# Optimization experiments

Measured on AMD Instinct MI355X. Metric: run time of the kernel, lower is better.

Reference implementation:

```python
import jax, jax.numpy as jnp
import numpy as np

B, T, I, H, L = 64, 512, 256, 512, 2


def setup_inputs() -> dict:
    key = jax.random.key(0)
    ks = jax.random.split(key, 9)
    std = 1.0 / np.sqrt(H)  # matches reset_parameters uniform(-std, std)
    u = lambda k, shape: jax.random.uniform(k, shape, jnp.float32, -std, std)
    return {
        "x": jax.random.normal(ks[0], (B, T, I), jnp.float32),
        "w_xh0": u(ks[1], (4 * H, I)),  "b_xh0": u(ks[2], (4 * H,)),
        "w_hh0": u(ks[3], (4 * H, H)), "b_hh0": u(ks[4], (4 * H,)),
        "w_xh1": u(ks[5], (4 * H, H)), "b_xh1": u(ks[6], (4 * H,)),
        "w_hh1": u(ks[7], (4 * H, H)), "b_hh1": u(ks[8], (4 * H,)),
    }


def _cell(x, h, c, Wx, bx, Wh, bh):
    # gates = xh(x) + hh(h); chunk order: input, forget, cell, output
    gates = x @ Wx.T + bx + h @ Wh.T + bh
    i, f, g, o = jnp.split(gates, 4, axis=1)
    cy = c * jax.nn.sigmoid(f) + jax.nn.sigmoid(i) * jnp.tanh(g)
    hy = jax.nn.sigmoid(o) * jnp.tanh(cy)
    return hy, cy


def reference(x, w_xh0, b_xh0, w_hh0, b_hh0, w_xh1, b_xh1, w_hh1, b_hh1):
    Bx, Tx, _ = x.shape
    Hx = w_hh0.shape[1]
    params = [(w_xh0, b_xh0, w_hh0, b_hh0), (w_xh1, b_xh1, w_hh1, b_hh1)]
    h0 = jnp.zeros((len(params), Bx, Hx), x.dtype)
    c0 = jnp.zeros((len(params), Bx, Hx), x.dtype)

    def step(carry, xt):
        h, c = carry
        inp = xt
        hs, cs = [], []
        for l, (Wx, bx, Wh, bh) in enumerate(params):
            hy, cy = _cell(inp, h[l], c[l], Wx, bx, Wh, bh)
            hs.append(hy)
            cs.append(cy)
            inp = hy  # dropout p=0.0 -> identity
        return (jnp.stack(hs), jnp.stack(cs)), inp

    (hT, cT), outs = jax.lax.scan(step, (h0, c0), jnp.swapaxes(x, 0, 1))
    return jnp.swapaxes(outs, 0, 1), (hT, cT)
```

## Files before the change

kernel.cpp:

```cpp
#include <hip/hip_runtime.h>
#include <stdint.h>

#define Bn 64
#define Tn 512
#define In 256
#define Hn 512
#define NBLK 64
#define OUT_HT 16777216
#define OUT_CT 16842752
#define LDS_BYTES 131072
#define SLOT_ELEMS (Bn * Hn)
#define DONE_WORDS (2 * 4 * Tn * 32)
#define DONE_BYTES (DONE_WORDS * 4)


typedef __attribute__((ext_vector_type(8))) short bf16x8;
typedef __attribute__((ext_vector_type(4))) float f32x4;
typedef unsigned long long u64;

__device__ __forceinline__ unsigned short f2bf(float f) {
    unsigned u = __float_as_uint(f);
    return (unsigned short)((u + 0x7fffu + ((u >> 16) & 1u)) >> 16);
}
__device__ __forceinline__ float sigm(float v) { return 1.0f / (1.0f + __expf(-v)); }
__device__ __forceinline__ float tanhv(float v) { float e = __expf(2.0f * v); return 1.0f - 2.0f / (e + 1.0f); }

__device__ __forceinline__ void stg_coh(unsigned short* p, unsigned short v) {
    __hip_atomic_store(p, v, __ATOMIC_RELAXED, __HIP_MEMORY_SCOPE_AGENT);
}
__device__ __forceinline__ int ld_cnt(const int* p) {
    return __hip_atomic_load(p, __ATOMIC_RELAXED, __HIP_MEMORY_SCOPE_AGENT);
}
__device__ __forceinline__ void st_flag(int* p, int v) {
    __hip_atomic_store(p, v, __ATOMIC_RELAXED, __HIP_MEMORY_SCOPE_AGENT);
}
__device__ __forceinline__ bf16x8 asbf(f32x4 v) {
    union { f32x4 f; bf16x8 h; } u; u.f = v; return u.h;
}

#define GLD16_ISSUE(A, VA)                                             \
  asm volatile(                                                        \
    "global_load_dwordx4 %0,  %16, off offset:0 sc0 sc1\n\t"          \
    "global_load_dwordx4 %1,  %16, off offset:64 sc0 sc1\n\t"         \
    "global_load_dwordx4 %2,  %16, off offset:128 sc0 sc1\n\t"        \
    "global_load_dwordx4 %3,  %16, off offset:192 sc0 sc1\n\t"        \
    "global_load_dwordx4 %4,  %16, off offset:256 sc0 sc1\n\t"        \
    "global_load_dwordx4 %5,  %16, off offset:320 sc0 sc1\n\t"        \
    "global_load_dwordx4 %6,  %16, off offset:384 sc0 sc1\n\t"        \
    "global_load_dwordx4 %7,  %16, off offset:448 sc0 sc1\n\t"        \
    "global_load_dwordx4 %8,  %16, off offset:512 sc0 sc1\n\t"        \
    "global_load_dwordx4 %9,  %16, off offset:576 sc0 sc1\n\t"        \
    "global_load_dwordx4 %10, %16, off offset:640 sc0 sc1\n\t"        \
    "global_load_dwordx4 %11, %16, off offset:704 sc0 sc1\n\t"        \
    "global_load_dwordx4 %12, %16, off offset:768 sc0 sc1\n\t"        \
    "global_load_dwordx4 %13, %16, off offset:832 sc0 sc1\n\t"        \
    "global_load_dwordx4 %14, %16, off offset:896 sc0 sc1\n\t"        \
    "global_load_dwordx4 %15, %16, off offset:960 sc0 sc1"             \
    : "=&v"(A[0]), "=&v"(A[1]), "=&v"(A[2]), "=&v"(A[3]),              \
      "=&v"(A[4]), "=&v"(A[5]), "=&v"(A[6]), "=&v"(A[7]),              \
      "=&v"(A[8]), "=&v"(A[9]), "=&v"(A[10]), "=&v"(A[11]),            \
      "=&v"(A[12]), "=&v"(A[13]), "=&v"(A[14]), "=&v"(A[15])           \
    : "v"(VA) : "memory")

#define VMW(n) do {                                                    \
    asm volatile("s_waitcnt vmcnt(" #n ")" ::: "memory");              \
    __builtin_amdgcn_sched_barrier(0);                                 \
  } while (0)

__global__ void lstm_prep(u64* __restrict__ z0, u64* __restrict__ z1,
                          int* __restrict__ dn) {
    int tid = blockIdx.x * blockDim.x + threadIdx.x;
    int stride = gridDim.x * blockDim.x;
    for (int i = tid; i < DONE_WORDS; i += stride) st_flag(dn + i, 0);
    for (int i = tid; i < SLOT_ELEMS / 4; i += stride) {
        __hip_atomic_store(z0 + i, (u64)0, __ATOMIC_RELAXED, __HIP_MEMORY_SCOPE_AGENT);
        __hip_atomic_store(z1 + i, (u64)0, __ATOMIC_RELAXED, __HIP_MEMORY_SCOPE_AGENT);
    }
}

__launch_bounds__(256, 1)
__global__ void lstm_main(const float* __restrict__ x,
                          const float* __restrict__ wxh0, const float* __restrict__ whh0,
                          const float* __restrict__ wxh1, const float* __restrict__ whh1,
                          const float* __restrict__ bx0, const float* __restrict__ bh0,
                          const float* __restrict__ bx1, const float* __restrict__ bh1,
                          float* __restrict__ out,
                          unsigned short* __restrict__ h0b,
                          unsigned short* __restrict__ h1b,
                          int* __restrict__ done, int nslot) {
    extern __shared__ char smem[];
    const int layer = blockIdx.x >> 5;
    const int cb    = blockIdx.x & 31;
    const int wv    = threadIdx.x >> 6;
    const int lane  = threadIdx.x & 63;
    const int quad  = lane >> 4;
    const int ln    = lane & 15;
    const int row0  = wv << 4;
    const int colh  = (cb << 4) + ln;

    const int I0 = (layer == 0) ? 8 : 16;
    const int K0 = (layer == 0) ? In : Hn;
    const float* Wxs = (layer == 0) ? wxh0 : wxh1;
    const float* Whs = (layer == 0) ? whh0 : whh1;
    u64* sm64 = (u64*)smem;
    const int tot0 = I0 * 4 * 64;
    for (int c = threadIdx.x; c < tot0; c += 256) {
        int lc = c & 63, qg = (c >> 6) & 3, ii = c >> 8;
        const float* src = Wxs + (size_t)(qg * Hn + (cb << 4) + (lc & 15)) * K0
                               + ii * 32 + (lc >> 4) * 8;
        f32x4 s0 = *(const f32x4*)src;
        f32x4 s1 = *(const f32x4*)(src + 4);
        u64 lo = (u64)f2bf(s0[0]) | ((u64)f2bf(s0[1]) << 16) |
                 ((u64)f2bf(s0[2]) << 32) | ((u64)f2bf(s0[3]) << 48);
        u64 hi = (u64)f2bf(s1[0]) | ((u64)f2bf(s1[1]) << 16) |
                 ((u64)f2bf(s1[2]) << 32) | ((u64)f2bf(s1[3]) << 48);
        sm64[c * 2] = lo; sm64[c * 2 + 1] = hi;
    }
    const int hbase = tot0;
    for (int c = threadIdx.x; c < 16 * 4 * 64; c += 256) {
        int lc = c & 63, qg = (c >> 6) & 3, ii = c >> 8;
        const float* src = Whs + (size_t)(qg * Hn + (cb << 4) + (lc & 15)) * Hn
                               + ii * 32 + (lc >> 4) * 8;
        f32x4 s0 = *(const f32x4*)src;
        f32x4 s1 = *(const f32x4*)(src + 4);
        u64 lo = (u64)f2bf(s0[0]) | ((u64)f2bf(s0[1]) << 16) |
                 ((u64)f2bf(s0[2]) << 32) | ((u64)f2bf(s0[3]) << 48);
        u64 hi = (u64)f2bf(s1[0]) | ((u64)f2bf(s1[1]) << 16) |
                 ((u64)f2bf(s1[2]) << 32) | ((u64)f2bf(s1[3]) << 48);
        sm64[(hbase + c) * 2] = lo; sm64[(hbase + c) * 2 + 1] = hi;
    }
    __syncthreads();
    const bf16x8* bfr = (const bf16x8*)smem;

    float bias[4];
#pragma unroll
    for (int q = 0; q < 4; ++q) {
        int gc = q * Hn + colh;
        bias[q] = (layer == 0) ? (bx0[gc] + bh0[gc]) : (bx1[gc] + bh1[gc]);
    }

    const float* xrow0 = x + (size_t)(row0 + ln) * Tn * In + quad * 8;
    const int hoff = (row0 + ln) * Hn + quad * 8;

    const int lm = lane & 31;
    const int* d0 = done + ((0 * 4 + wv) * Tn) * 32 + lm;
    const int* d1 = done + ((1 * 4 + wv) * Tn) * 32 + lm;
    int* pub = done + ((layer * 4 + wv) * Tn) * 32 + cb;

    float c[4] = {0.f, 0.f, 0.f, 0.f};
    int rs = 0, wsl = 1;
    int gdone = -1;

    for (int t = 0; t < Tn; ++t) {
        f32x4 acc[4];
#pragma unroll
        for (int q = 0; q < 4; ++q) acc[q] = (f32x4){bias[q], bias[q], bias[q], bias[q]};

        if (layer == 0) {
            const float* xp = xrow0 + (size_t)t * In;
            f32x4 xr[16];
#pragma unroll
            for (int i = 0; i < 8; ++i) {
                xr[2 * i]     = *(const f32x4*)(xp + i * 32);
                xr[2 * i + 1] = *(const f32x4*)(xp + i * 32 + 4);
            }
            bf16x8 axc[8];
#pragma unroll
            for (int i = 0; i < 8; ++i) {
                f32x4 xa = xr[2 * i], xc = xr[2 * i + 1];
                axc[i][0] = (short)f2bf(xa[0]); axc[i][1] = (short)f2bf(xa[1]);
                axc[i][2] = (short)f2bf(xa[2]); axc[i][3] = (short)f2bf(xa[3]);
                axc[i][4] = (short)f2bf(xc[0]); axc[i][5] = (short)f2bf(xc[1]);
                axc[i][6] = (short)f2bf(xc[2]); axc[i][7] = (short)f2bf(xc[3]);
            }
#pragma unroll
            for (int i = 0; i < 8; ++i)
#pragma unroll
                for (int q = 0; q < 4; ++q)
                    acc[q] = __builtin_amdgcn_mfma_f32_16x16x32_bf16(
                        axc[i], bfr[(i * 4 + q) * 64 + lane], acc[q], 0, 0, 0);

            {
                int g = t + 1 - nslot;
                if (g >= 0 && g > gdone) {
                    int probe = g + 32; if (probe > Tn - 1) probe = Tn - 1;
                    if (__all(ld_cnt(d1 + probe * 32) > 0)) gdone = probe;
                    else {
                        const int* gp = d1 + g * 32;
                        while (!__all(ld_cnt(gp) > 0)) __builtin_amdgcn_s_sleep(4);
                        gdone = g;
                    }
                }
            }
            if (t > 0) {
                const int* p = d0 + (t - 1) * 32;
                while (!__all(ld_cnt(p) > 0)) { }
            }
            asm volatile("" ::: "memory");

            const unsigned short* hp = h0b + (size_t)rs * SLOT_ELEMS + hoff;
            f32x4 A[16];
            uint64_t va = (uint64_t)hp;
            GLD16_ISSUE(A, va);
            VMW(12);
#pragma unroll
            for (int i = 0; i < 4; ++i)
#pragma unroll
                for (int q = 0; q < 4; ++q)
                    acc[q] = __builtin_amdgcn_mfma_f32_16x16x32_bf16(
                        asbf(A[i]), bfr[hbase + (i * 4 + q) * 64 + lane], acc[q], 0, 0, 0);
            VMW(8);
#pragma unroll
            for (int i = 4; i < 8; ++i)
#pragma unroll
                for (int q = 0; q < 4; ++q)
                    acc[q] = __builtin_amdgcn_mfma_f32_16x16x32_bf16(
                        asbf(A[i]), bfr[hbase + (i * 4 + q) * 64 + lane], acc[q], 0, 0, 0);
            VMW(4);
#pragma unroll
            for (int i = 8; i < 12; ++i)
#pragma unroll
                for (int q = 0; q < 4; ++q)
                    acc[q] = __builtin_amdgcn_mfma_f32_16x16x32_bf16(
                        asbf(A[i]), bfr[hbase + (i * 4 + q) * 64 + lane], acc[q], 0, 0, 0);
            VMW(0);
#pragma unroll
            for (int i = 12; i < 16; ++i)
#pragma unroll
                for (int q = 0; q < 4; ++q)
                    acc[q] = __builtin_amdgcn_mfma_f32_16x16x32_bf16(
                        asbf(A[i]), bfr[hbase + (i * 4 + q) * 64 + lane], acc[q], 0, 0, 0);
        } else {
            {
                const int* p = d0 + t * 32;
                while (!__all(ld_cnt(p) > 0)) { }
            }
            asm volatile("" ::: "memory");
            const unsigned short* p0 = h0b + (size_t)wsl * SLOT_ELEMS + hoff;
            f32x4 A[16], Bv[16];
            uint64_t va = (uint64_t)p0;
            GLD16_ISSUE(A, va);
            if (t > 0) {
                const int* p = d1 + (t - 1) * 32;
                while (!__all(ld_cnt(p) > 0)) { }
            }
            asm volatile("" ::: "memory");
            const unsigned short* p1 = h1b + (size_t)rs * SLOT_ELEMS + hoff;
            uint64_t vb = (uint64_t)p1;
            GLD16_ISSUE(Bv, vb);
            VMW(28);
#pragma unroll
            for (int i = 0; i < 4; ++i)
#pragma unroll
                for (int q = 0; q < 4; ++q)
                    acc[q] = __builtin_amdgcn_mfma_f32_16x16x32_bf16(
                        asbf(A[i]), bfr[(i * 4 + q) * 64 + lane], acc[q], 0, 0, 0);
            VMW(24);
#pragma unroll
            for (int i = 4; i < 8; ++i)
#pragma unroll
                for (int q = 0; q < 4; ++q)
                    acc[q] = __builtin_amdgcn_mfma_f32_16x16x32_bf16(
                        asbf(A[i]), bfr[(i * 4 + q) * 64 + lane], acc[q], 0, 0, 0);
            VMW(20);
#pragma unroll
            for (int i = 8; i < 12; ++i)
#pragma unroll
                for (int q = 0; q < 4; ++q)
                    acc[q] = __builtin_amdgcn_mfma_f32_16x16x32_bf16(
                        asbf(A[i]), bfr[(i * 4 + q) * 64 + lane], acc[q], 0, 0, 0);
            VMW(16);
#pragma unroll
            for (int i = 12; i < 16; ++i)
#pragma unroll
                for (int q = 0; q < 4; ++q)
                    acc[q] = __builtin_amdgcn_mfma_f32_16x16x32_bf16(
                        asbf(A[i]), bfr[(i * 4 + q) * 64 + lane], acc[q], 0, 0, 0);
            VMW(12);
#pragma unroll
            for (int i = 0; i < 4; ++i)
#pragma unroll
                for (int q = 0; q < 4; ++q)
                    acc[q] = __builtin_amdgcn_mfma_f32_16x16x32_bf16(
                        asbf(Bv[i]), bfr[hbase + (i * 4 + q) * 64 + lane], acc[q], 0, 0, 0);
            VMW(8);
#pragma unroll
            for (int i = 4; i < 8; ++i)
#pragma unroll
                for (int q = 0; q < 4; ++q)
                    acc[q] = __builtin_amdgcn_mfma_f32_16x16x32_bf16(
                        asbf(Bv[i]), bfr[hbase + (i * 4 + q) * 64 + lane], acc[q], 0, 0, 0);
            VMW(4);
#pragma unroll
            for (int i = 8; i < 12; ++i)
#pragma unroll
                for (int q = 0; q < 4; ++q)
                    acc[q] = __builtin_amdgcn_mfma_f32_16x16x32_bf16(
                        asbf(Bv[i]), bfr[hbase + (i * 4 + q) * 64 + lane], acc[q], 0, 0, 0);
            VMW(0);
#pragma unroll
            for (int i = 12; i < 16; ++i)
#pragma unroll
                for (int q = 0; q < 4; ++q)
                    acc[q] = __builtin_amdgcn_mfma_f32_16x16x32_bf16(
                        asbf(Bv[i]), bfr[hbase + (i * 4 + q) * 64 + lane], acc[q], 0, 0, 0);
        }

        unsigned short* hw = ((layer == 0) ? h0b : h1b) + (size_t)wsl * SLOT_ELEMS;
        float hv[4];
#pragma unroll
        for (int r = 0; r < 4; ++r) {
            int row = row0 + quad * 4 + r;
            float ig = sigm(acc[0][r]);
            float fg = sigm(acc[1][r]);
            float gg = tanhv(acc[2][r]);
            float og = sigm(acc[3][r]);
            float cy = c[r] * fg + ig * gg;
            float hy = og * tanhv(cy);
            c[r] = cy;
            hv[r] = hy;
            stg_coh(hw + row * Hn + colh, f2bf(hy));
        }
        asm volatile("s_waitcnt vmcnt(0)" ::: "memory");
        if (lane == 0) st_flag(pub + t * 32, t + 1);

        if (layer == 1) {
#pragma unroll
            for (int r = 0; r < 4; ++r) {
                int row = row0 + quad * 4 + r;
                out[(size_t)row * (Tn * Hn) + (size_t)t * Hn + colh] = hv[r];
            }
        }
        if (t == Tn - 1) {
#pragma unroll
            for (int r = 0; r < 4; ++r) {
                int row = row0 + quad * 4 + r;
                out[OUT_HT + layer * (Bn * Hn) + row * Hn + colh] = hv[r];
                out[OUT_CT + layer * (Bn * Hn) + row * Hn + colh] = c[r];
            }
        }

        rs = wsl;
        wsl = (wsl + 1 == nslot) ? 0 : wsl + 1;
    }
}

extern "C" void kernel_launch(void* const* d_in, const int* in_sizes, int n_in,
                              void* d_out, int out_size, void* d_ws, size_t ws_size,
                              hipStream_t stream) {
    const float* x    = (const float*)d_in[0];
    const float* wxh0 = (const float*)d_in[1];
    const float* bxh0 = (const float*)d_in[2];
    const float* whh0 = (const float*)d_in[3];
    const float* bhh0 = (const float*)d_in[4];
    const float* wxh1 = (const float*)d_in[5];
    const float* bxh1 = (const float*)d_in[6];
    const float* whh1 = (const float*)d_in[7];
    const float* bhh1 = (const float*)d_in[8];
    float* out = (float*)d_out;

    char* ws = (char*)d_ws;
    int* done = (int*)ws;
    long nslot_l = (long)((ws_size - DONE_BYTES) / (2 * (size_t)SLOT_ELEMS * 2));
    int nslot = (int)(nslot_l < 3 ? 3 : (nslot_l > Tn + 1 ? Tn + 1 : nslot_l));
    unsigned short* h0b = (unsigned short*)(ws + DONE_BYTES);
    unsigned short* h1b = h0b + (size_t)nslot * SLOT_ELEMS;

    static int lds_attr_set = 0;
    if (!lds_attr_set) {
        hipFuncSetAttribute((const void*)lstm_main,
                            hipFuncAttributeMaxDynamicSharedMemorySize, LDS_BYTES);
        lds_attr_set = 1;
    }

    lstm_prep<<<dim3(256), dim3(256), 0, stream>>>((u64*)h0b, (u64*)h1b, done);

    lstm_main<<<dim3(NBLK), dim3(256), LDS_BYTES, stream>>>(
        x, wxh0, whh0, wxh1, whh1, bxh0, bhh0, bxh1, bhh1,
        out, h0b, h1b, done, nslot);
}
```

Measured before the change: 3.365 ms.

## Replace per-step flag handshakes with sentinel-filled hidden-state slots polled directly

Adds a canary path. A prep kernel fills every per-timestep hidden-state slot (except slot 0) with a bf16 NaN sentinel. Consumer warps then load the h data directly and retry until no sentinel halfword remains, checked with packed u16 min reductions. This drops the separate done-flag publish and poll round trip on each recurrent step, which should shorten the serial critical path. In exchange it needs a full workspace of T+1 slots per layer and a large fill pass before the main kernel. It keeps the old flag-based kernel as a fallback when the workspace is too small.

```diff
diff --git a/kernel.cpp b/kernel.cpp
--- a/kernel.cpp
+++ b/kernel.cpp
@@ -12,6 +12,8 @@
 #define SLOT_ELEMS (Bn * Hn)
 #define DONE_WORDS (2 * 4 * Tn * 32)
 #define DONE_BYTES (DONE_WORDS * 4)
+#define NSLOT_CAN (Tn + 1)
+#define MAX_RETRY (1 << 20)
 
 
 typedef __attribute__((ext_vector_type(8))) short bf16x8;
@@ -36,6 +38,11 @@
 }
 __device__ __forceinline__ bf16x8 asbf(f32x4 v) {
     union { f32x4 f; bf16x8 h; } u; u.f = v; return u.h;
+}
+__device__ __forceinline__ unsigned pkminu16(unsigned a, unsigned b) {
+    unsigned d;
+    asm("v_pk_min_u16 %0, %1, %2" : "=v"(d) : "v"(a), "v"(b));
+    return d;
 }
 
 #define GLD16_ISSUE(A, VA)                                             \
@@ -62,32 +69,114 @@
       "=&v"(A[12]), "=&v"(A[13]), "=&v"(A[14]), "=&v"(A[15])           \
     : "v"(VA) : "memory")
 
+#define GLD16X(A, VA)                                                  \
+  asm volatile(                                                        \
+    "global_load_dwordx4 %0,  %16, off offset:0\n\t"                   \
+    "global_load_dwordx4 %1,  %16, off offset:16\n\t"                  \
+    "global_load_dwordx4 %2,  %16, off offset:128\n\t"                 \
+    "global_load_dwordx4 %3,  %16, off offset:144\n\t"                 \
+    "global_load_dwordx4 %4,  %16, off offset:256\n\t"                 \
+    "global_load_dwordx4 %5,  %16, off offset:272\n\t"                 \
+    "global_load_dwordx4 %6,  %16, off offset:384\n\t"                 \
+    "global_load_dwordx4 %7,  %16, off offset:400\n\t"                 \
+    "global_load_dwordx4 %8,  %16, off offset:512\n\t"                 \
+    "global_load_dwordx4 %9,  %16, off offset:528\n\t"                 \
+    "global_load_dwordx4 %10, %16, off offset:640\n\t"                 \
+    "global_load_dwordx4 %11, %16, off offset:656\n\t"                 \
+    "global_load_dwordx4 %12, %16, off offset:768\n\t"                 \
+    "global_load_dwordx4 %13, %16, off offset:784\n\t"                 \
+    "global_load_dwordx4 %14, %16, off offset:896\n\t"                 \
+    "global_load_dwordx4 %15, %16, off offset:912"                     \
+    : "=&v"(A[0]), "=&v"(A[1]), "=&v"(A[2]), "=&v"(A[3]),              \
+      "=&v"(A[4]), "=&v"(A[5]), "=&v"(A[6]), "=&v"(A[7]),              \
+      "=&v"(A[8]), "=&v"(A[9]), "=&v"(A[10]), "=&v"(A[11]),            \
+      "=&v"(A[12]), "=&v"(A[13]), "=&v"(A[14]), "=&v"(A[15])           \
+    : "v"(VA) : "memory")
+
 #define VMW(n) do {                                                    \
     asm volatile("s_waitcnt vmcnt(" #n ")" ::: "memory");              \
     __builtin_amdgcn_sched_barrier(0);                                 \
   } while (0)
 
+#define CANCHK(A, OK) do {                                             \
+    unsigned m0_ = 0xFFFFFFFFu, m1_ = 0xFFFFFFFFu,                     \
+             m2_ = 0xFFFFFFFFu, m3_ = 0xFFFFFFFFu;                     \
+    _Pragma("unroll")                                                  \
+    for (int i_ = 0; i_ < 16; ++i_) {                                  \
+      m0_ = pkminu16(m0_, __float_as_uint(A[i_][0]) ^ 0x7FC17FC1u);    \
+      m1_ = pkminu16(m1_, __float_as_uint(A[i_][1]) ^ 0x7FC17FC1u);    \
+      m2_ = pkminu16(m2_, __float_as_uint(A[i_][2]) ^ 0x7FC17FC1u);    \
+      m3_ = pkminu16(m3_, __float_as_uint(A[i_][3]) ^ 0x7FC17FC1u);    \
+    }                                                                  \
+    unsigned mt_ = pkminu16(pkminu16(m0_, m1_), pkminu16(m2_, m3_));   \
+    OK = __all(((mt_ & 0xFFFFu) != 0u) && ((mt_ >> 16) != 0u));        \
+  } while (0)
+
 __global__ void lstm_prep(u64* __restrict__ z0, u64* __restrict__ z1,
-                          int* __restrict__ dn) {
-    int tid = blockIdx.x * blockDim.x + threadIdx.x;
-    int stride = gridDim.x * blockDim.x;
-    for (int i = tid; i < DONE_WORDS; i += stride) st_flag(dn + i, 0);
-    for (int i = tid; i < SLOT_ELEMS / 4; i += stride) {
-        __hip_atomic_store(z0 + i, (u64)0, __ATOMIC_RELAXED, __HIP_MEMORY_SCOPE_AGENT);
-        __hip_atomic_store(z1 + i, (u64)0, __ATOMIC_RELAXED, __HIP_MEMORY_SCOPE_AGENT);
-    }
-}
+                          int* __restrict__ dn, int mode) {
+    long tid = (long)blockIdx.x * blockDim.x + threadIdx.x;
+    long stride = (long)gridDim.x * blockDim.x;
+    if (mode == 0) {
+        for (long i = tid; i < DONE_WORDS; i += stride) st_flag(dn + i, 0);
+        for (long i = tid; i < SLOT_ELEMS / 4; i += stride) {
+            __hip_atomic_store(z0 + i, (u64)0, __ATOMIC_RELAXED, __HIP_MEMORY_SCOPE_AGENT);
+            __hip_atomic_store(z1 + i, (u64)0, __ATOMIC_RELAXED, __HIP_MEMORY_SCOPE_AGENT);
+        }
+    } else {
+        const u64 CAN = 0x7FC17FC17FC17FC1ull;
+        const long N = (long)NSLOT_CAN * (SLOT_ELEMS / 4);
+        for (long i = tid; i < N; i += stride) {
+            u64 v = (i < SLOT_ELEMS / 4) ? 0ull : CAN;
+            __hip_atomic_store(z0 + i, v, __ATOMIC_RELAXED, __HIP_MEMORY_SCOPE_AGENT);
+            __hip_atomic_store(z1 + i, v, __ATOMIC_RELAXED, __HIP_MEMORY_SCOPE_AGENT);
+        }
+    }
+}
+
+#define STAGE_WEIGHTS()                                                      \
+    const int I0 = (layer == 0) ? 8 : 16;                                    \
+    const int K0 = (layer == 0) ? In : Hn;                                   \
+    const float* Wxs = (layer == 0) ? wxh0 : wxh1;                           \
+    const float* Whs = (layer == 0) ? whh0 : whh1;                           \
+    u64* sm64 = (u64*)smem;                                                  \
+    const int tot0 = I0 * 4 * 64;                                            \
+    for (int c = threadIdx.x; c < tot0; c += 256) {                          \
+        int lc = c & 63, qg = (c >> 6) & 3, ii = c >> 8;                     \
+        const float* src = Wxs + (size_t)(qg * Hn + (cb << 4) + (lc & 15)) * K0 \
+                               + ii * 32 + (lc >> 4) * 8;                    \
+        f32x4 s0 = *(const f32x4*)src;                                       \
+        f32x4 s1 = *(const f32x4*)(src + 4);                                 \
+        u64 lo = (u64)f2bf(s0[0]) | ((u64)f2bf(s0[1]) << 16) |               \
+                 ((u64)f2bf(s0[2]) << 32) | ((u64)f2bf(s0[3]) << 48);        \
+        u64 hi = (u64)f2bf(s1[0]) | ((u64)f2bf(s1[1]) << 16) |               \
+                 ((u64)f2bf(s1[2]) << 32) | ((u64)f2bf(s1[3]) << 48);        \
+        sm64[c * 2] = lo; sm64[c * 2 + 1] = hi;                              \
+    }                                                                        \
+    const int hbase = tot0;                                                  \
+    for (int c = threadIdx.x; c < 16 * 4 * 64; c += 256) {                   \
+        int lc = c & 63, qg = (c >> 6) & 3, ii = c >> 8;                     \
+        const float* src = Whs + (size_t)(qg * Hn + (cb << 4) + (lc & 15)) * Hn \
+                               + ii * 32 + (lc >> 4) * 8;                    \
+        f32x4 s0 = *(const f32x4*)src;                                       \
+        f32x4 s1 = *(const f32x4*)(src + 4);                                 \
+        u64 lo = (u64)f2bf(s0[0]) | ((u64)f2bf(s0[1]) << 16) |               \
+                 ((u64)f2bf(s0[2]) << 32) | ((u64)f2bf(s0[3]) << 48);        \
+        u64 hi = (u64)f2bf(s1[0]) | ((u64)f2bf(s1[1]) << 16) |               \
+                 ((u64)f2bf(s1[2]) << 32) | ((u64)f2bf(s1[3]) << 48);        \
+        sm64[(hbase + c) * 2] = lo; sm64[(hbase + c) * 2 + 1] = hi;          \
+    }                                                                        \
+    __syncthreads();                                                         \
+    const bf16x8* bfr = (const bf16x8*)smem;
 
 __launch_bounds__(256, 1)
-__global__ void lstm_main(const float* __restrict__ x,
-                          const float* __restrict__ wxh0, const float* __restrict__ whh0,
-                          const float* __restrict__ wxh1, const float* __restrict__ whh1,
-                          const float* __restrict__ bx0, const float* __restrict__ bh0,
-                          const float* __restrict__ bx1, const float* __restrict__ bh1,
-                          float* __restrict__ out,
-                          unsigned short* __restrict__ h0b,
-                          unsigned short* __restrict__ h1b,
-                          int* __restrict__ done, int nslot) {
+__global__ void lstm_canary(const float* __restrict__ x,
+                            const float* __restrict__ wxh0, const float* __restrict__ whh0,
+                            const float* __restrict__ wxh1, const float* __restrict__ whh1,
+                            const float* __restrict__ bx0, const float* __restrict__ bh0,
+                            const float* __restrict__ bx1, const float* __restrict__ bh1,
+                            float* __restrict__ out,
+                            unsigned short* __restrict__ h0b,
+                            unsigned short* __restrict__ h1b) {
     extern __shared__ char smem[];
     const int layer = blockIdx.x >> 5;
     const int cb    = blockIdx.x & 31;
@@ -98,39 +187,147 @@
     const int row0  = wv << 4;
     const int colh  = (cb << 4) + ln;
 
-    const int I0 = (layer == 0) ? 8 : 16;
-    const int K0 = (layer == 0) ? In : Hn;
-    const float* Wxs = (layer == 0) ? wxh0 : wxh1;
-    const float* Whs = (layer == 0) ? whh0 : whh1;
-    u64* sm64 = (u64*)smem;
-    const int tot0 = I0 * 4 * 64;
-    for (int c = threadIdx.x; c < tot0; c += 256) {
-        int lc = c & 63, qg = (c >> 6) & 3, ii = c >> 8;
-        const float* src = Wxs + (size_t)(qg * Hn + (cb << 4) + (lc & 15)) * K0
-                               + ii * 32 + (lc >> 4) * 8;
-        f32x4 s0 = *(const f32x4*)src;
-        f32x4 s1 = *(const f32x4*)(src + 4);
-        u64 lo = (u64)f2bf(s0[0]) | ((u64)f2bf(s0[1]) << 16) |
-                 ((u64)f2bf(s0[2]) << 32) | ((u64)f2bf(s0[3]) << 48);
-        u64 hi = (u64)f2bf(s1[0]) | ((u64)f2bf(s1[1]) << 16) |
-                 ((u64)f2bf(s1[2]) << 32) | ((u64)f2bf(s1[3]) << 48);
-        sm64[c * 2] = lo; sm64[c * 2 + 1] = hi;
-    }
-    const int hbase = tot0;
-    for (int c = threadIdx.x; c < 16 * 4 * 64; c += 256) {
-        int lc = c & 63, qg = (c >> 6) & 3, ii = c >> 8;
-        const float* src = Whs + (size_t)(qg * Hn + (cb << 4) + (lc & 15)) * Hn
-                               + ii * 32 + (lc >> 4) * 8;
-        f32x4 s0 = *(const f32x4*)src;
-        f32x4 s1 = *(const f32x4*)(src + 4);
-        u64 lo = (u64)f2bf(s0[0]) | ((u64)f2bf(s0[1]) << 16) |
-                 ((u64)f2bf(s0[2]) << 32) | ((u64)f2bf(s0[3]) << 48);
-        u64 hi = (u64)f2bf(s1[0]) | ((u64)f2bf(s1[1]) << 16) |
-                 ((u64)f2bf(s1[2]) << 32) | ((u64)f2bf(s1[3]) << 48);
-        sm64[(hbase + c) * 2] = lo; sm64[(hbase + c) * 2 + 1] = hi;
-    }
-    __syncthreads();
-    const bf16x8* bfr = (const bf16x8*)smem;
+    STAGE_WEIGHTS();
+
+    float bias[4];
+#pragma unroll
+    for (int q = 0; q < 4; ++q) {
+        int gc = q * Hn + colh;
+        bias[q] = (layer == 0) ? (bx0[gc] + bh0[gc]) : (bx1[gc] + bh1[gc]);
+    }
+
+    const float* xrow0 = x + (size_t)(row0 + ln) * Tn * In + quad * 8;
+    const int hoff = (row0 + ln) * Hn + quad * 8;
+
+    float c[4] = {0.f, 0.f, 0.f, 0.f};
+
+    for (int t = 0; t < Tn; ++t) {
+        f32x4 acc[4];
+#pragma unroll
+        for (int q = 0; q < 4; ++q) acc[q] = (f32x4){bias[q], bias[q], bias[q], bias[q]};
+
+        if (layer == 0) {
+            const unsigned short* hp = h0b + (size_t)t * SLOT_ELEMS + hoff;
+            uint64_t va = (uint64_t)hp;
+            f32x4 A[16], xr[16];
+            uint64_t vax = (uint64_t)(xrow0 + (size_t)t * In);
+            GLD16_ISSUE(A, va);
+            GLD16X(xr, vax);
+            VMW(16);
+            int ok; CANCHK(A, ok);
+            int tries = 0;
+            while (!ok && ++tries < MAX_RETRY) {
+                GLD16_ISSUE(A, va); VMW(0); CANCHK(A, ok);
+            }
+#pragma unroll
+            for (int i = 0; i < 16; ++i)
+#pragma unroll
+                for (int q = 0; q < 4; ++q)
+                    acc[q] = __builtin_amdgcn_mfma_f32_16x16x32_bf16(
+                        asbf(A[i]), bfr[hbase + (i * 4 + q) * 64 + lane], acc[q], 0, 0, 0);
+            VMW(0);
+            bf16x8 axc[8];
+#pragma unroll
+            for (int i = 0; i < 8; ++i) {
+                f32x4 xa = xr[2 * i], xc = xr[2 * i + 1];
+                axc[i][0] = (short)f2bf(xa[0]); axc[i][1] = (short)f2bf(xa[1]);
+                axc[i][2] = (short)f2bf(xa[2]); axc[i][3] = (short)f2bf(xa[3]);
+                axc[i][4] = (short)f2bf(xc[0]); axc[i][5] = (short)f2bf(xc[1]);
+                axc[i][6] = (short)f2bf(xc[2]); axc[i][7] = (short)f2bf(xc[3]);
+            }
+#pragma unroll
+            for (int i = 0; i < 8; ++i)
+#pragma unroll
+                for (int q = 0; q < 4; ++q)
+                    acc[q] = __builtin_amdgcn_mfma_f32_16x16x32_bf16(
+                        axc[i], bfr[(i * 4 + q) * 64 + lane], acc[q], 0, 0, 0);
+        } else {
+            const unsigned short* p0 = h0b + (size_t)(t + 1) * SLOT_ELEMS + hoff;
+            const unsigned short* p1 = h1b + (size_t)t * SLOT_ELEMS + hoff;
+            uint64_t va = (uint64_t)p0, vb = (uint64_t)p1;
+            f32x4 A[16], Bv[16];
+            GLD16_ISSUE(A, va);
+            GLD16_ISSUE(Bv, vb);
+            VMW(16);
+            int ok; CANCHK(A, ok);
+            int tries = 0;
+            while (!ok && ++tries < MAX_RETRY) {
+                GLD16_ISSUE(A, va); VMW(0); CANCHK(A, ok);
+            }
+#pragma unroll
+            for (int i = 0; i < 16; ++i)
+#pragma unroll
+                for (int q = 0; q < 4; ++q)
+                    acc[q] = __builtin_amdgcn_mfma_f32_16x16x32_bf16(
+                        asbf(A[i]), bfr[(i * 4 + q) * 64 + lane], acc[q], 0, 0, 0);
+            VMW(0);
+            CANCHK(Bv, ok);
+            tries = 0;
+            while (!ok && ++tries < MAX_RETRY) {
+                GLD16_ISSUE(Bv, vb); VMW(0); CANCHK(Bv, ok);
+            }
+#pragma unroll
+            for (int i = 0; i < 16; ++i)
+#pragma unroll
+                for (int q = 0; q < 4; ++q)
+                    acc[q] = __builtin_amdgcn_mfma_f32_16x16x32_bf16(
+                        asbf(Bv[i]), bfr[hbase + (i * 4 + q) * 64 + lane], acc[q], 0, 0, 0);
+        }
+
+        unsigned short* hw = ((layer == 0) ? h0b : h1b) + (size_t)(t + 1) * SLOT_ELEMS;
+        float hv[4];
+#pragma unroll
+        for (int r = 0; r < 4; ++r) {
+            int row = row0 + quad * 4 + r;
+            float ig = sigm(acc[0][r]);
+            float fg = sigm(acc[1][r]);
+            float gg = tanhv(acc[2][r]);
+            float og = sigm(acc[3][r]);
+            float cy = c[r] * fg + ig * gg;
+            float hy = og * tanhv(cy);
+            c[r] = cy;
+            hv[r] = hy;
+            stg_coh(hw + row * Hn + colh, f2bf(hy));
+        }
+        if (layer == 1) {
+#pragma unroll
+            for (int r = 0; r < 4; ++r) {
+                int row = row0 + quad * 4 + r;
+                out[(size_t)row * (Tn * Hn) + (size_t)t * Hn + colh] = hv[r];
+            }
+        }
+        if (t == Tn - 1) {
+#pragma unroll
+            for (int r = 0; r < 4; ++r) {
+                int row = row0 + quad * 4 + r;
+                out[OUT_HT + layer * (Bn * Hn) + row * Hn + colh] = hv[r];
+                out[OUT_CT + layer * (Bn * Hn) + row * Hn + colh] = c[r];
+            }
+        }
+    }
+}
+
+__launch_bounds__(256, 1)
+__global__ void lstm_flags(const float* __restrict__ x,
+                           const float* __restrict__ wxh0, const float* __restrict__ whh0,
+                           const float* __restrict__ wxh1, const float* __restrict__ whh1,
+                           const float* __restrict__ bx0, const float* __restrict__ bh0,
+                           const float* __restrict__ bx1, const float* __restrict__ bh1,
+                           float* __restrict__ out,
+                           unsigned short* __restrict__ h0b,
+                           unsigned short* __restrict__ h1b,
+                           int* __restrict__ done, int nslot) {
+    extern __shared__ char smem[];
+    const int layer = blockIdx.x >> 5;
+    const int cb    = blockIdx.x & 31;
+    const int wv    = threadIdx.x >> 6;
+    const int lane  = threadIdx.x & 63;
+    const int quad  = lane >> 4;
+    const int ln    = lane & 15;
+    const int row0  = wv << 4;
+    const int colh  = (cb << 4) + ln;
+
+    STAGE_WEIGHTS();
 
     float bias[4];
 #pragma unroll
@@ -361,21 +558,33 @@
 
     char* ws = (char*)d_ws;
     int* done = (int*)ws;
-    long nslot_l = (long)((ws_size - DONE_BYTES) / (2 * (size_t)SLOT_ELEMS * 2));
-    int nslot = (int)(nslot_l < 3 ? 3 : (nslot_l > Tn + 1 ? Tn + 1 : nslot_l));
     unsigned short* h0b = (unsigned short*)(ws + DONE_BYTES);
-    unsigned short* h1b = h0b + (size_t)nslot * SLOT_ELEMS;
 
     static int lds_attr_set = 0;
     if (!lds_attr_set) {
-        hipFuncSetAttribute((const void*)lstm_main,
+        hipFuncSetAttribute((const void*)lstm_canary,
+                            hipFuncAttributeMaxDynamicSharedMemorySize, LDS_BYTES);
+        hipFuncSetAttribute((const void*)lstm_flags,
                             hipFuncAttributeMaxDynamicSharedMemorySize, LDS_BYTES);
         lds_attr_set = 1;
     }
 
-    lstm_prep<<<dim3(256), dim3(256), 0, stream>>>((u64*)h0b, (u64*)h1b, done);
-
-    lstm_main<<<dim3(NBLK), dim3(256), LDS_BYTES, stream>>>(
-        x, wxh0, whh0, wxh1, whh1, bxh0, bhh0, bxh1, bhh1,
-        out, h0b, h1b, done, nslot);
-}
+    const size_t need_can = (size_t)DONE_BYTES
+                          + 2ull * NSLOT_CAN * SLOT_ELEMS * 2 + 64;
+    if (ws_size >= need_can) {
+        unsigned short* h1b = h0b + (size_t)NSLOT_CAN * SLOT_ELEMS;
+        lstm_prep<<<dim3(1024), dim3(256), 0, stream>>>(
+            (u64*)h0b, (u64*)h1b, done, 1);
+        lstm_canary<<<dim3(NBLK), dim3(256), LDS_BYTES, stream>>>(
+            x, wxh0, whh0, wxh1, whh1, bxh0, bhh0, bxh1, bhh1, out, h0b, h1b);
+    } else {
+        long nslot_l = (long)((ws_size - DONE_BYTES) / (2 * (size_t)SLOT_ELEMS * 2));
+        int nslot = (int)(nslot_l < 3 ? 3 : (nslot_l > Tn + 1 ? Tn + 1 : nslot_l));
+        unsigned short* h1b = h0b + (size_t)nslot * SLOT_ELEMS;
+        lstm_prep<<<dim3(256), dim3(256), 0, stream>>>(
+            (u64*)h0b, (u64*)h1b, done, 0);
+        lstm_flags<<<dim3(NBLK), dim3(256), LDS_BYTES, stream>>>(
+            x, wxh0, whh0, wxh1, whh1, bxh0, bhh0, bxh1, bhh1,
+            out, h0b, h1b, done, nslot);
+    }
+}
```

Result: slower. 3.562 ms (+5.9%).
